# Kernel optimization log

Hardware: AMD Instinct MI355X
Metric: run time of the kernel (lower is better)

Reference implementation:

```python
import jax, jax.numpy as jnp
import numpy as np

N = 100_000   # number of sparse points
C = 128       # channels
K3 = 27       # 3x3x3 kernel offsets


def sparse_conv(x, nbr, W, b):
    """Minkowski-style sparse conv: gather-GEMM-scatter.
    x:   [N, Cin] point features
    nbr: [N, K3] neighbor index per kernel offset; index N -> missing (zero row)
    W:   [K3, Cin, Cout], b: [Cout]
    """
    x_pad = jnp.concatenate([x, jnp.zeros((1, x.shape[1]), x.dtype)], axis=0)

    def step(acc, wk_nk):
        Wk, nk = wk_nk                      # Wk: [Cin,Cout], nk: [N]
        return acc + x_pad[nk] @ Wk, None   # gather + GEMM, accumulate

    acc0 = jnp.broadcast_to(b, (x.shape[0], W.shape[2])).astype(x.dtype)
    acc, _ = jax.lax.scan(step, acc0, (W, nbr.T))
    return acc


def setup_inputs() -> dict:
    key = jax.random.key(0)
    ks = jax.random.split(key, 12)
    Ch = C // 2

    def w(k, shape, fan_in):
        return jax.random.normal(k, shape, dtype=jnp.float32) / np.sqrt(fan_in)

    x = jax.random.normal(ks[0], (N, C), dtype=jnp.float32)
    # neighbor map; value N means "no neighbor" (maps to zero-padded row)
    nbr = jax.random.randint(ks[1], (N, K3), 0, N + 1, dtype=jnp.int32)

    return {
        "x": x,
        "nbr": nbr,
        "W00": w(ks[2], (K3, C, Ch), K3 * C),   # conv0_0: kxkxk, C -> C/2
        "b00": jnp.zeros((Ch,), jnp.float32),
        "W01": w(ks[3], (K3, Ch, Ch), K3 * Ch),  # conv0_1: kxkxk, C/2 -> C/2
        "b01": jnp.zeros((Ch,), jnp.float32),
        "W10": w(ks[4], (C, Ch), C),             # conv1_0: 1x1x1, C -> C/2
        "b10": jnp.zeros((Ch,), jnp.float32),
        "W11": w(ks[5], (K3, Ch, Ch), K3 * Ch),  # conv1_1: kxkxk, C/2 -> C/2
        "b11": jnp.zeros((Ch,), jnp.float32),
        "W12": w(ks[6], (Ch, Ch), Ch),           # conv1_2: 1x1x1, C/2 -> C/2
        "b12": jnp.zeros((Ch,), jnp.float32),
    }


def reference(x, nbr, W00, b00, W01, b01, W10, b10, W11, b11, W12, b12):
    # branch 0: conv -> relu -> conv
    h0 = jax.nn.relu(sparse_conv(x, nbr, W00, b00))
    out0 = sparse_conv(h0, nbr, W01, b01)
    # branch 1: 1x1 conv -> relu -> conv -> relu -> 1x1 conv
    h1 = jax.nn.relu(x @ W10 + b10)
    h1 = jax.nn.relu(sparse_conv(h1, nbr, W11, b11))
    out1 = h1 @ W12 + b12
    # concat channels, residual add
    return jnp.concatenate([out0, out1], axis=1) + x
```

## Files before the change

### kernel.cpp

```cpp
#include <hip/hip_runtime.h>
#include <hip/hip_bf16.h>
#include <stdint.h>

typedef __bf16 bf16x8 __attribute__((ext_vector_type(8)));
typedef float  f32x4  __attribute__((ext_vector_type(4)));

#define MFMA(A, B, C) __builtin_amdgcn_mfma_f32_16x16x32_bf16((A), (B), (C), 0, 0, 0)

static __device__ __forceinline__ unsigned short f2b(float f) {
    union { float f; unsigned int u; } v; v.f = f;
    return (unsigned short)((v.u + 0x7FFFu + ((v.u >> 16) & 1u)) >> 16);
}

static __device__ __forceinline__ bf16x8 perm_frag(int sel, bf16x8 D) {
    union { bf16x8 v; int d[4]; } u, r;
    u.v = D;
#pragma unroll
    for (int w = 0; w < 4; ++w) r.d[w] = __builtin_amdgcn_ds_bpermute(sel, u.d[w]);
    return r.v;
}

__global__ __launch_bounds__(256) void convert_kernel(
    const float* __restrict__ x, unsigned short* __restrict__ xb,
    unsigned short* __restrict__ hb, int N) {
    long long i = (long long)blockIdx.x * blockDim.x + threadIdx.x;
    long long base = i * 4;
    long long nx = (long long)N * 128;
    long long total = nx + 128;
    if (base >= total) return;
    if (base < nx) {
        float4 v = *(const float4*)(x + base);
        ushort4 o;
        o.x = f2b(v.x); o.y = f2b(v.y); o.z = f2b(v.z); o.w = f2b(v.w);
        *(ushort4*)(xb + base) = o;
    } else {
        ushort4 z = make_ushort4(0, 0, 0, 0);
        *(ushort4*)(xb + base) = z;
        *(ushort4*)(hb + base) = z;
    }
}

__global__ __launch_bounds__(256) void pack_kernel(
    const float* __restrict__ W00, const float* __restrict__ W01,
    const float* __restrict__ W10, const float* __restrict__ W11,
    const float* __restrict__ W12,
    unsigned short* __restrict__ wp00, unsigned short* __restrict__ wpC,
    unsigned short* __restrict__ wp10, unsigned short* __restrict__ wp12) {
    int g = blockIdx.x * blockDim.x + threadIdx.x;
    const float* W; int cinSteps; int which;
    if (g < 27648)      { W = W00; cinSteps = 4; which = 0; }
    else if (g < 41472) { g -= 27648; W = W01; cinSteps = 2; which = 1; }
    else if (g < 55296) { g -= 41472; W = W11; cinSteps = 2; which = 2; }
    else if (g < 56320) { g -= 55296; W = W10; cinSteps = 4; which = 3; }
    else if (g < 56832) { g -= 56320; W = W12; cinSteps = 2; which = 4; }
    else return;
    int lane = g & 63;
    int st   = g >> 6;
    int t    = st & 3;
    int s    = st >> 2;
    int q = lane >> 4, n16 = lane & 15;
    int k    = s / cinSteps;
    int cinb = (s % cinSteps) * 32;
    int Cin  = cinSteps * 32;
    int cout = t * 16 + n16;
    unsigned short o[8];
#pragma unroll
    for (int j = 0; j < 8; ++j) {
        float v = W[(size_t)(k * Cin + cinb + q * 8 + j) * 64 + cout];
        o[j] = f2b(v);
    }
    unsigned short* dst;
    if (which == 0)      dst = wp00 + (size_t)g * 8;
    else if (which == 1) dst = wpC + (size_t)k * 8192 +
                               ((size_t)(((s & 1) * 4 + t) * 64 + lane)) * 8;
    else if (which == 2) dst = wpC + (size_t)k * 8192 + 4096 +
                               ((size_t)(((s & 1) * 4 + t) * 64 + lane)) * 8;
    else if (which == 3) dst = wp10 + (size_t)g * 8;
    else                 dst = wp12 + (size_t)g * 8;
    *(ushort4*)(dst)     = make_ushort4(o[0], o[1], o[2], o[3]);
    *(ushort4*)(dst + 4) = make_ushort4(o[4], o[5], o[6], o[7]);
}

__global__ __launch_bounds__(256, 2) void passB_kernel(
    const unsigned short* __restrict__ xb, const int* __restrict__ nbr,
    const unsigned short* __restrict__ wp00, const unsigned short* __restrict__ wp10,
    const float* __restrict__ b00, const float* __restrict__ b10,
    unsigned short* __restrict__ hb, int N) {
    __shared__ __align__(16) unsigned short bbuf[2][8192];
    __shared__ int lds_idx[128 * 27];
    int tid = threadIdx.x;
    int lane = tid & 63;
    int wv   = tid >> 6;
    int q = lane >> 4, n16 = lane & 15;
    int rowq = lane >> 2, chunk = lane & 3;
    int sel = (n16 * 4 + q) * 4;
    int rowbase = blockIdx.x * 128 + wv * 32;

    {
        long long gbase = (long long)blockIdx.x * 128 * 27;
        long long lim = (long long)N * 27 - 1;
        for (int i = tid; i < 3456; i += 256) {
            long long gi = gbase + i; if (gi > lim) gi = lim;
            lds_idx[i] = nbr[gi];
        }
    }
    int4 br[4];
#pragma unroll
    for (int j = 0; j < 4; ++j) br[j] = *(const int4*)(wp00 + j * 2048 + tid * 8);
#pragma unroll
    for (int j = 0; j < 4; ++j) *(int4*)(&bbuf[0][j * 2048 + tid * 8]) = br[j];
    __syncthreads();

    f32x4 acc0[2][4];
    f32x4 acc1[2][4];
#pragma unroll
    for (int rs = 0; rs < 2; ++rs)
#pragma unroll
        for (int t = 0; t < 4; ++t) { acc0[rs][t] = (f32x4)0.f; acc1[rs][t] = (f32x4)0.f; }

    int idxb0 = (wv * 32 + rowq) * 27;
    int idxb1 = (wv * 32 + 16 + rowq) * 27;
    int own0 = min(rowbase + rowq, N - 1);
    int own1 = min(rowbase + 16 + rowq, N - 1);

    int ia = lds_idx[idxb0], ib = lds_idx[idxb1];
    bf16x8 D0[4], D1[4];
    {
        const unsigned short* p0 = xb + (size_t)ia * 128 + chunk * 8;
        const unsigned short* p1 = xb + (size_t)ib * 128 + chunk * 8;
#pragma unroll
        for (int s2 = 0; s2 < 4; ++s2) {
            D0[s2] = *(const bf16x8*)(p0 + s2 * 32);
            D1[s2] = *(const bf16x8*)(p1 + s2 * 32);
        }
    }

    for (int k = 0; k < 27; ++k) {
        int buf = k & 1;
        if (k < 26) {
            const unsigned short* src = wp00 + (size_t)(k + 1) * 8192;
#pragma unroll
            for (int j = 0; j < 4; ++j) br[j] = *(const int4*)(src + j * 2048 + tid * 8);
        }
        int ian = (k + 1 < 27) ? lds_idx[idxb0 + k + 1] : own0;
        int ibn = (k + 1 < 27) ? lds_idx[idxb1 + k + 1] : own1;
        bf16x8 D0n[4], D1n[4];
        {
            const unsigned short* p0 = xb + (size_t)ian * 128 + chunk * 8;
            const unsigned short* p1 = xb + (size_t)ibn * 128 + chunk * 8;
#pragma unroll
            for (int s2 = 0; s2 < 4; ++s2) {
                D0n[s2] = *(const bf16x8*)(p0 + s2 * 32);
                D1n[s2] = *(const bf16x8*)(p1 + s2 * 32);
            }
        }
        const unsigned short* lb = &bbuf[buf][0];
#pragma unroll
        for (int s2 = 0; s2 < 4; ++s2) {
            bf16x8 A0 = perm_frag(sel, D0[s2]);
            bf16x8 A1 = perm_frag(sel, D1[s2]);
#pragma unroll
            for (int t = 0; t < 4; ++t) {
                bf16x8 B = *(const bf16x8*)(lb + (s2 * 4 + t) * 512 + lane * 8);
                acc0[0][t] = MFMA(A0, B, acc0[0][t]);
                acc0[1][t] = MFMA(A1, B, acc0[1][t]);
            }
        }
        if (k < 26) {
#pragma unroll
            for (int j = 0; j < 4; ++j)
                *(int4*)(&bbuf[buf ^ 1][j * 2048 + tid * 8]) = br[j];
        }
#pragma unroll
        for (int s2 = 0; s2 < 4; ++s2) { D0[s2] = D0n[s2]; D1[s2] = D1n[s2]; }
        __syncthreads();
    }

#pragma unroll
    for (int s2 = 0; s2 < 4; ++s2) {
        bf16x8 A0 = perm_frag(sel, D0[s2]);
        bf16x8 A1 = perm_frag(sel, D1[s2]);
#pragma unroll
        for (int t = 0; t < 4; ++t) {
            bf16x8 B = *(const bf16x8*)(wp10 + s2 * 2048 + t * 512 + lane * 8);
            acc1[0][t] = MFMA(A0, B, acc1[0][t]);
            acc1[1][t] = MFMA(A1, B, acc1[1][t]);
        }
    }

#pragma unroll
    for (int rs = 0; rs < 2; ++rs)
#pragma unroll
        for (int t = 0; t < 4; ++t) {
            int col = t * 16 + n16;
            float bb0 = b00[col], bb1 = b10[col];
#pragma unroll
            for (int r = 0; r < 4; ++r) {
                int row = rowbase + rs * 16 + q * 4 + r;
                if (row < N) {
                    hb[(size_t)row * 128 + col]      = f2b(fmaxf(acc0[rs][t][r] + bb0, 0.f));
                    hb[(size_t)row * 128 + 64 + col] = f2b(fmaxf(acc1[rs][t][r] + bb1, 0.f));
                }
            }
        }
}

__global__ __launch_bounds__(256, 2) void passC_kernel(
    const unsigned short* __restrict__ hb, const int* __restrict__ nbr,
    const float* __restrict__ x,
    const unsigned short* __restrict__ wpC, const unsigned short* __restrict__ wp12,
    const float* __restrict__ b01, const float* __restrict__ b11,
    const float* __restrict__ b12, float* __restrict__ out, int N) {
    __shared__ __align__(16) unsigned short bbuf[2][8192];
    __shared__ int lds_idx[128 * 27];
    int tid = threadIdx.x;
    int lane = tid & 63;
    int wv   = tid >> 6;
    int q = lane >> 4, n16 = lane & 15;
    int rowq = lane >> 2, chunk = lane & 3;
    int sel = (n16 * 4 + q) * 4;
    int rowbase = blockIdx.x * 128 + wv * 32;

    {
        long long gbase = (long long)blockIdx.x * 128 * 27;
        long long lim = (long long)N * 27 - 1;
        for (int i = tid; i < 3456; i += 256) {
            long long gi = gbase + i; if (gi > lim) gi = lim;
            lds_idx[i] = nbr[gi];
        }
    }
    int4 br[4];
#pragma unroll
    for (int j = 0; j < 4; ++j) br[j] = *(const int4*)(wpC + j * 2048 + tid * 8);
#pragma unroll
    for (int j = 0; j < 4; ++j) *(int4*)(&bbuf[0][j * 2048 + tid * 8]) = br[j];
    __syncthreads();

    f32x4 accO0[2][4];
    f32x4 accT[2][4];
#pragma unroll
    for (int rs = 0; rs < 2; ++rs)
#pragma unroll
        for (int t = 0; t < 4; ++t) { accO0[rs][t] = (f32x4)0.f; accT[rs][t] = (f32x4)0.f; }

    int idxb0 = (wv * 32 + rowq) * 27;
    int idxb1 = (wv * 32 + 16 + rowq) * 27;

    int ia = lds_idx[idxb0], ib = lds_idx[idxb1];
    bf16x8 DA0[2], DC0[2], DA1[2], DC1[2];
    {
        const unsigned short* p0 = hb + (size_t)ia * 128 + chunk * 8;
        const unsigned short* p1 = hb + (size_t)ib * 128 + chunk * 8;
#pragma unroll
        for (int s2 = 0; s2 < 2; ++s2) {
            DA0[s2] = *(const bf16x8*)(p0 + s2 * 32);
            DC0[s2] = *(const bf16x8*)(p0 + 64 + s2 * 32);
            DA1[s2] = *(const bf16x8*)(p1 + s2 * 32);
            DC1[s2] = *(const bf16x8*)(p1 + 64 + s2 * 32);
        }
    }

    for (int k = 0; k < 27; ++k) {
        int buf = k & 1;
        if (k < 26) {
            const unsigned short* src = wpC + (size_t)(k + 1) * 8192;
#pragma unroll
            for (int j = 0; j < 4; ++j) br[j] = *(const int4*)(src + j * 2048 + tid * 8);
        }
        bf16x8 DA0n[2], DC0n[2], DA1n[2], DC1n[2];
        if (k < 26) {
            int ian = lds_idx[idxb0 + k + 1];
            int ibn = lds_idx[idxb1 + k + 1];
            const unsigned short* p0 = hb + (size_t)ian * 128 + chunk * 8;
            const unsigned short* p1 = hb + (size_t)ibn * 128 + chunk * 8;
#pragma unroll
            for (int s2 = 0; s2 < 2; ++s2) {
                DA0n[s2] = *(const bf16x8*)(p0 + s2 * 32);
                DC0n[s2] = *(const bf16x8*)(p0 + 64 + s2 * 32);
                DA1n[s2] = *(const bf16x8*)(p1 + s2 * 32);
                DC1n[s2] = *(const bf16x8*)(p1 + 64 + s2 * 32);
            }
        }
        const unsigned short* lb = &bbuf[buf][0];
#pragma unroll
        for (int s2 = 0; s2 < 2; ++s2) {
            bf16x8 A0 = perm_frag(sel, DA0[s2]);
            bf16x8 A1 = perm_frag(sel, DA1[s2]);
#pragma unroll
            for (int t = 0; t < 4; ++t) {
                bf16x8 B = *(const bf16x8*)(lb + (s2 * 4 + t) * 512 + lane * 8);
                accO0[0][t] = MFMA(A0, B, accO0[0][t]);
                accO0[1][t] = MFMA(A1, B, accO0[1][t]);
            }
            bf16x8 C0 = perm_frag(sel, DC0[s2]);
            bf16x8 C1 = perm_frag(sel, DC1[s2]);
#pragma unroll
            for (int t = 0; t < 4; ++t) {
                bf16x8 B2 = *(const bf16x8*)(lb + 4096 + (s2 * 4 + t) * 512 + lane * 8);
                accT[0][t] = MFMA(C0, B2, accT[0][t]);
                accT[1][t] = MFMA(C1, B2, accT[1][t]);
            }
        }
        if (k < 26) {
#pragma unroll
            for (int j = 0; j < 4; ++j)
                *(int4*)(&bbuf[buf ^ 1][j * 2048 + tid * 8]) = br[j];
#pragma unroll
            for (int s2 = 0; s2 < 2; ++s2) {
                DA0[s2] = DA0n[s2]; DC0[s2] = DC0n[s2];
                DA1[s2] = DA1n[s2]; DC1[s2] = DC1n[s2];
            }
        }
        __syncthreads();
    }

    unsigned short* scratch = &bbuf[0][0];
    unsigned short* myl = scratch + wv * 2304;
#pragma unroll
    for (int rs = 0; rs < 2; ++rs)
#pragma unroll
        for (int t = 0; t < 4; ++t) {
            int col = t * 16 + n16;
            float bo = b01[col], bt = b11[col];
#pragma unroll
            for (int r = 0; r < 4; ++r) {
                int row = rowbase + rs * 16 + q * 4 + r;
                if (row < N) {
                    float xv = __builtin_nontemporal_load(x + (size_t)row * 128 + col);
                    __builtin_nontemporal_store(accO0[rs][t][r] + bo + xv,
                                                out + (size_t)row * 128 + col);
                }
                float tv = fmaxf(accT[rs][t][r] + bt, 0.f);
                myl[(rs * 16 + q * 4 + r) * 72 + col] = f2b(tv);
            }
        }

    f32x4 accO1[2][4];
#pragma unroll
    for (int rs = 0; rs < 2; ++rs)
#pragma unroll
        for (int t = 0; t < 4; ++t) accO1[rs][t] = (f32x4)0.f;
#pragma unroll
    for (int s2 = 0; s2 < 2; ++s2) {
        bf16x8 A0 = *(const bf16x8*)(myl + n16 * 72 + s2 * 32 + q * 8);
        bf16x8 A1 = *(const bf16x8*)(myl + (16 + n16) * 72 + s2 * 32 + q * 8);
#pragma unroll
        for (int t = 0; t < 4; ++t) {
            bf16x8 B = *(const bf16x8*)(wp12 + s2 * 2048 + t * 512 + lane * 8);
            accO1[0][t] = MFMA(A0, B, accO1[0][t]);
            accO1[1][t] = MFMA(A1, B, accO1[1][t]);
        }
    }
#pragma unroll
    for (int rs = 0; rs < 2; ++rs)
#pragma unroll
        for (int t = 0; t < 4; ++t) {
            int col = t * 16 + n16;
            float bo = b12[col];
#pragma unroll
            for (int r = 0; r < 4; ++r) {
                int row = rowbase + rs * 16 + q * 4 + r;
                if (row < N) {
                    float xv = __builtin_nontemporal_load(x + (size_t)row * 128 + 64 + col);
                    __builtin_nontemporal_store(accO1[rs][t][r] + bo + xv,
                                                out + (size_t)row * 128 + 64 + col);
                }
            }
        }
}

extern "C" void kernel_launch(void* const* d_in, const int* in_sizes, int n_in,
                              void* d_out, int out_size, void* d_ws, size_t ws_size,
                              hipStream_t stream) {
    const float* x   = (const float*)d_in[0];
    const int*   nbr = (const int*)d_in[1];
    const float* W00 = (const float*)d_in[2];
    const float* b00 = (const float*)d_in[3];
    const float* W01 = (const float*)d_in[4];
    const float* b01 = (const float*)d_in[5];
    const float* W10 = (const float*)d_in[6];
    const float* b10 = (const float*)d_in[7];
    const float* W11 = (const float*)d_in[8];
    const float* b11 = (const float*)d_in[9];
    const float* W12 = (const float*)d_in[10];
    const float* b12 = (const float*)d_in[11];
    float* out = (float*)d_out;
    int N = in_sizes[0] / 128;

    char* ws = (char*)d_ws;
    size_t cur = 0;
    unsigned short* xb  = (unsigned short*)(ws + cur); cur += (size_t)(N + 1) * 128 * 2;
    unsigned short* hb  = (unsigned short*)(ws + cur); cur += (size_t)(N + 1) * 128 * 2;
    unsigned short* wp00 = (unsigned short*)(ws + cur); cur += 27648 * 8 * 2;
    unsigned short* wpC  = (unsigned short*)(ws + cur); cur += (size_t)27 * 8192 * 2;
    unsigned short* wp10 = (unsigned short*)(ws + cur); cur += 8192 * 2;
    unsigned short* wp12 = (unsigned short*)(ws + cur); cur += 4096 * 2;

    long long cvt_groups = ((long long)N * 128 + 128) / 4;
    int cvt_blocks = (int)((cvt_groups + 255) / 256);
    convert_kernel<<<cvt_blocks, 256, 0, stream>>>(x, xb, hb, N);
    pack_kernel<<<222, 256, 0, stream>>>(W00, W01, W10, W11, W12,
                                         wp00, wpC, wp10, wp12);
    int blocks = (N + 127) / 128;
    passB_kernel<<<blocks, 256, 0, stream>>>(xb, nbr, wp00, wp10, b00, b10, hb, N);
    passC_kernel<<<blocks, 256, 0, stream>>>(hb, nbr, x, wpC, wp12,
                                             b01, b11, b12, out, N);
}
```

Before: 414.3 us.

## Convert gather-GEMM passes to persistent blocks with atomic strip scheduling

Both conv passes now launch a fixed grid of 768 persistent blocks that pull 128-row strips from a global atomic counter, instead of one block per strip. The in-loop __syncthreads is also replaced with an explicit lgkmcnt wait plus s_barrier, so the barrier no longer waits on outstanding global loads. The aim is to cut block launch and tail overhead and to overlap the gather prefetch with the barrier. In exchange it adds an atomic and an extra barrier per strip, and it reloads the first weight slice for every strip.

```diff
diff --git a/kernel.cpp b/kernel.cpp
--- a/kernel.cpp
+++ b/kernel.cpp
@@ -6,6 +6,8 @@
 typedef float  f32x4  __attribute__((ext_vector_type(4)));
 
 #define MFMA(A, B, C) __builtin_amdgcn_mfma_f32_16x16x32_bf16((A), (B), (C), 0, 0, 0)
+
+#define LDS_BARRIER() asm volatile("s_waitcnt lgkmcnt(0)\n\ts_barrier" ::: "memory")
 
 static __device__ __forceinline__ unsigned short f2b(float f) {
     union { float f; unsigned int u; } v; v.f = f;
@@ -85,124 +87,133 @@
     const unsigned short* __restrict__ xb, const int* __restrict__ nbr,
     const unsigned short* __restrict__ wp00, const unsigned short* __restrict__ wp10,
     const float* __restrict__ b00, const float* __restrict__ b10,
-    unsigned short* __restrict__ hb, int N) {
+    unsigned short* __restrict__ hb, int N, int* __restrict__ ctr, int nstrips) {
     __shared__ __align__(16) unsigned short bbuf[2][8192];
     __shared__ int lds_idx[128 * 27];
+    __shared__ int sstrip;
     int tid = threadIdx.x;
     int lane = tid & 63;
     int wv   = tid >> 6;
     int q = lane >> 4, n16 = lane & 15;
     int rowq = lane >> 2, chunk = lane & 3;
     int sel = (n16 * 4 + q) * 4;
-    int rowbase = blockIdx.x * 128 + wv * 32;
-
-    {
-        long long gbase = (long long)blockIdx.x * 128 * 27;
-        long long lim = (long long)N * 27 - 1;
-        for (int i = tid; i < 3456; i += 256) {
-            long long gi = gbase + i; if (gi > lim) gi = lim;
-            lds_idx[i] = nbr[gi];
-        }
-    }
-    int4 br[4];
-#pragma unroll
-    for (int j = 0; j < 4; ++j) br[j] = *(const int4*)(wp00 + j * 2048 + tid * 8);
-#pragma unroll
-    for (int j = 0; j < 4; ++j) *(int4*)(&bbuf[0][j * 2048 + tid * 8]) = br[j];
-    __syncthreads();
-
-    f32x4 acc0[2][4];
-    f32x4 acc1[2][4];
-#pragma unroll
-    for (int rs = 0; rs < 2; ++rs)
-#pragma unroll
-        for (int t = 0; t < 4; ++t) { acc0[rs][t] = (f32x4)0.f; acc1[rs][t] = (f32x4)0.f; }
-
-    int idxb0 = (wv * 32 + rowq) * 27;
-    int idxb1 = (wv * 32 + 16 + rowq) * 27;
-    int own0 = min(rowbase + rowq, N - 1);
-    int own1 = min(rowbase + 16 + rowq, N - 1);
-
-    int ia = lds_idx[idxb0], ib = lds_idx[idxb1];
-    bf16x8 D0[4], D1[4];
-    {
-        const unsigned short* p0 = xb + (size_t)ia * 128 + chunk * 8;
-        const unsigned short* p1 = xb + (size_t)ib * 128 + chunk * 8;
-#pragma unroll
-        for (int s2 = 0; s2 < 4; ++s2) {
-            D0[s2] = *(const bf16x8*)(p0 + s2 * 32);
-            D1[s2] = *(const bf16x8*)(p1 + s2 * 32);
-        }
-    }
-
-    for (int k = 0; k < 27; ++k) {
-        int buf = k & 1;
-        if (k < 26) {
-            const unsigned short* src = wp00 + (size_t)(k + 1) * 8192;
-#pragma unroll
-            for (int j = 0; j < 4; ++j) br[j] = *(const int4*)(src + j * 2048 + tid * 8);
-        }
-        int ian = (k + 1 < 27) ? lds_idx[idxb0 + k + 1] : own0;
-        int ibn = (k + 1 < 27) ? lds_idx[idxb1 + k + 1] : own1;
-        bf16x8 D0n[4], D1n[4];
+
+    for (;;) {
+        if (tid == 0) sstrip = atomicAdd(ctr, 1);
+        __syncthreads();
+        int strip = sstrip;
+        if (strip >= nstrips) break;
+        int rowbase = strip * 128 + wv * 32;
+
+        int4 br[4];
+#pragma unroll
+        for (int j = 0; j < 4; ++j) br[j] = *(const int4*)(wp00 + j * 2048 + tid * 8);
         {
-            const unsigned short* p0 = xb + (size_t)ian * 128 + chunk * 8;
-            const unsigned short* p1 = xb + (size_t)ibn * 128 + chunk * 8;
+            long long gbase = (long long)strip * 128 * 27;
+            long long lim = (long long)N * 27 - 1;
+            for (int i = tid; i < 3456; i += 256) {
+                long long gi = gbase + i; if (gi > lim) gi = lim;
+                lds_idx[i] = nbr[gi];
+            }
+        }
+#pragma unroll
+        for (int j = 0; j < 4; ++j) *(int4*)(&bbuf[0][j * 2048 + tid * 8]) = br[j];
+        __syncthreads();
+
+        f32x4 acc0[2][4];
+        f32x4 acc1[2][4];
+#pragma unroll
+        for (int rs = 0; rs < 2; ++rs)
+#pragma unroll
+            for (int t = 0; t < 4; ++t) { acc0[rs][t] = (f32x4)0.f; acc1[rs][t] = (f32x4)0.f; }
+
+        int idxb0 = (wv * 32 + rowq) * 27;
+        int idxb1 = (wv * 32 + 16 + rowq) * 27;
+        int own0 = min(rowbase + rowq, N - 1);
+        int own1 = min(rowbase + 16 + rowq, N - 1);
+
+        int ia = lds_idx[idxb0], ib = lds_idx[idxb1];
+        bf16x8 D0[4], D1[4];
+        {
+            const unsigned short* p0 = xb + (size_t)ia * 128 + chunk * 8;
+            const unsigned short* p1 = xb + (size_t)ib * 128 + chunk * 8;
 #pragma unroll
             for (int s2 = 0; s2 < 4; ++s2) {
-                D0n[s2] = *(const bf16x8*)(p0 + s2 * 32);
-                D1n[s2] = *(const bf16x8*)(p1 + s2 * 32);
-            }
-        }
-        const unsigned short* lb = &bbuf[buf][0];
+                D0[s2] = *(const bf16x8*)(p0 + s2 * 32);
+                D1[s2] = *(const bf16x8*)(p1 + s2 * 32);
+            }
+        }
+
+        for (int k = 0; k < 27; ++k) {
+            int buf = k & 1;
+            if (k < 26) {
+                const unsigned short* src = wp00 + (size_t)(k + 1) * 8192;
+#pragma unroll
+                for (int j = 0; j < 4; ++j) br[j] = *(const int4*)(src + j * 2048 + tid * 8);
+            }
+            int ian = (k + 1 < 27) ? lds_idx[idxb0 + k + 1] : own0;
+            int ibn = (k + 1 < 27) ? lds_idx[idxb1 + k + 1] : own1;
+            bf16x8 D0n[4], D1n[4];
+            {
+                const unsigned short* p0 = xb + (size_t)ian * 128 + chunk * 8;
+                const unsigned short* p1 = xb + (size_t)ibn * 128 + chunk * 8;
+#pragma unroll
+                for (int s2 = 0; s2 < 4; ++s2) {
+                    D0n[s2] = *(const bf16x8*)(p0 + s2 * 32);
+                    D1n[s2] = *(const bf16x8*)(p1 + s2 * 32);
+                }
+            }
+            const unsigned short* lb = &bbuf[buf][0];
+#pragma unroll
+            for (int s2 = 0; s2 < 4; ++s2) {
+                bf16x8 A0 = perm_frag(sel, D0[s2]);
+                bf16x8 A1 = perm_frag(sel, D1[s2]);
+#pragma unroll
+                for (int t = 0; t < 4; ++t) {
+                    bf16x8 B = *(const bf16x8*)(lb + (s2 * 4 + t) * 512 + lane * 8);
+                    acc0[0][t] = MFMA(A0, B, acc0[0][t]);
+                    acc0[1][t] = MFMA(A1, B, acc0[1][t]);
+                }
+            }
+            if (k < 26) {
+#pragma unroll
+                for (int j = 0; j < 4; ++j)
+                    *(int4*)(&bbuf[buf ^ 1][j * 2048 + tid * 8]) = br[j];
+            }
+#pragma unroll
+            for (int s2 = 0; s2 < 4; ++s2) { D0[s2] = D0n[s2]; D1[s2] = D1n[s2]; }
+            LDS_BARRIER();
+        }
+
 #pragma unroll
         for (int s2 = 0; s2 < 4; ++s2) {
             bf16x8 A0 = perm_frag(sel, D0[s2]);
             bf16x8 A1 = perm_frag(sel, D1[s2]);
 #pragma unroll
             for (int t = 0; t < 4; ++t) {
-                bf16x8 B = *(const bf16x8*)(lb + (s2 * 4 + t) * 512 + lane * 8);
-                acc0[0][t] = MFMA(A0, B, acc0[0][t]);
-                acc0[1][t] = MFMA(A1, B, acc0[1][t]);
-            }
-        }
-        if (k < 26) {
-#pragma unroll
-            for (int j = 0; j < 4; ++j)
-                *(int4*)(&bbuf[buf ^ 1][j * 2048 + tid * 8]) = br[j];
-        }
-#pragma unroll
-        for (int s2 = 0; s2 < 4; ++s2) { D0[s2] = D0n[s2]; D1[s2] = D1n[s2]; }
+                bf16x8 B = *(const bf16x8*)(wp10 + s2 * 2048 + t * 512 + lane * 8);
+                acc1[0][t] = MFMA(A0, B, acc1[0][t]);
+                acc1[1][t] = MFMA(A1, B, acc1[1][t]);
+            }
+        }
+
+#pragma unroll
+        for (int rs = 0; rs < 2; ++rs)
+#pragma unroll
+            for (int t = 0; t < 4; ++t) {
+                int col = t * 16 + n16;
+                float bb0 = b00[col], bb1 = b10[col];
+#pragma unroll
+                for (int r = 0; r < 4; ++r) {
+                    int row = rowbase + rs * 16 + q * 4 + r;
+                    if (row < N) {
+                        hb[(size_t)row * 128 + col]      = f2b(fmaxf(acc0[rs][t][r] + bb0, 0.f));
+                        hb[(size_t)row * 128 + 64 + col] = f2b(fmaxf(acc1[rs][t][r] + bb1, 0.f));
+                    }
+                }
+            }
         __syncthreads();
     }
-
-#pragma unroll
-    for (int s2 = 0; s2 < 4; ++s2) {
-        bf16x8 A0 = perm_frag(sel, D0[s2]);
-        bf16x8 A1 = perm_frag(sel, D1[s2]);
-#pragma unroll
-        for (int t = 0; t < 4; ++t) {
-            bf16x8 B = *(const bf16x8*)(wp10 + s2 * 2048 + t * 512 + lane * 8);
-            acc1[0][t] = MFMA(A0, B, acc1[0][t]);
-            acc1[1][t] = MFMA(A1, B, acc1[1][t]);
-        }
-    }
-
-#pragma unroll
-    for (int rs = 0; rs < 2; ++rs)
-#pragma unroll
-        for (int t = 0; t < 4; ++t) {
-            int col = t * 16 + n16;
-            float bb0 = b00[col], bb1 = b10[col];
-#pragma unroll
-            for (int r = 0; r < 4; ++r) {
-                int row = rowbase + rs * 16 + q * 4 + r;
-                if (row < N) {
-                    hb[(size_t)row * 128 + col]      = f2b(fmaxf(acc0[rs][t][r] + bb0, 0.f));
-                    hb[(size_t)row * 128 + 64 + col] = f2b(fmaxf(acc1[rs][t][r] + bb1, 0.f));
-                }
-            }
-        }
 }
 
 __global__ __launch_bounds__(256, 2) void passC_kernel(
@@ -210,163 +221,173 @@
     const float* __restrict__ x,
     const unsigned short* __restrict__ wpC, const unsigned short* __restrict__ wp12,
     const float* __restrict__ b01, const float* __restrict__ b11,
-    const float* __restrict__ b12, float* __restrict__ out, int N) {
+    const float* __restrict__ b12, float* __restrict__ out, int N,
+    int* __restrict__ ctr, int nstrips) {
     __shared__ __align__(16) unsigned short bbuf[2][8192];
     __shared__ int lds_idx[128 * 27];
+    __shared__ int sstrip;
     int tid = threadIdx.x;
     int lane = tid & 63;
     int wv   = tid >> 6;
     int q = lane >> 4, n16 = lane & 15;
     int rowq = lane >> 2, chunk = lane & 3;
     int sel = (n16 * 4 + q) * 4;
-    int rowbase = blockIdx.x * 128 + wv * 32;
-
-    {
-        long long gbase = (long long)blockIdx.x * 128 * 27;
-        long long lim = (long long)N * 27 - 1;
-        for (int i = tid; i < 3456; i += 256) {
-            long long gi = gbase + i; if (gi > lim) gi = lim;
-            lds_idx[i] = nbr[gi];
-        }
+
+    for (;;) {
+        if (tid == 0) sstrip = atomicAdd(ctr, 1);
+        __syncthreads();
+        int strip = sstrip;
+        if (strip >= nstrips) break;
+        int rowbase = strip * 128 + wv * 32;
+
+        int4 br[4];
+#pragma unroll
+        for (int j = 0; j < 4; ++j) br[j] = *(const int4*)(wpC + j * 2048 + tid * 8);
+        {
+            long long gbase = (long long)strip * 128 * 27;
+            long long lim = (long long)N * 27 - 1;
+            for (int i = tid; i < 3456; i += 256) {
+                long long gi = gbase + i; if (gi > lim) gi = lim;
+                lds_idx[i] = nbr[gi];
+            }
+        }
+#pragma unroll
+        for (int j = 0; j < 4; ++j) *(int4*)(&bbuf[0][j * 2048 + tid * 8]) = br[j];
+        __syncthreads();
+
+        f32x4 accO0[2][4];
+        f32x4 accT[2][4];
+#pragma unroll
+        for (int rs = 0; rs < 2; ++rs)
+#pragma unroll
+            for (int t = 0; t < 4; ++t) { accO0[rs][t] = (f32x4)0.f; accT[rs][t] = (f32x4)0.f; }
+
+        int idxb0 = (wv * 32 + rowq) * 27;
+        int idxb1 = (wv * 32 + 16 + rowq) * 27;
+
+        int ia = lds_idx[idxb0], ib = lds_idx[idxb1];
+        bf16x8 DA0[2], DC0[2], DA1[2], DC1[2];
+        {
+            const unsigned short* p0 = hb + (size_t)ia * 128 + chunk * 8;
+            const unsigned short* p1 = hb + (size_t)ib * 128 + chunk * 8;
+#pragma unroll
+            for (int s2 = 0; s2 < 2; ++s2) {
+                DA0[s2] = *(const bf16x8*)(p0 + s2 * 32);
+                DC0[s2] = *(const bf16x8*)(p0 + 64 + s2 * 32);
+                DA1[s2] = *(const bf16x8*)(p1 + s2 * 32);
+                DC1[s2] = *(const bf16x8*)(p1 + 64 + s2 * 32);
+            }
+        }
+
+        for (int k = 0; k < 27; ++k) {
+            int buf = k & 1;
+            if (k < 26) {
+                const unsigned short* src = wpC + (size_t)(k + 1) * 8192;
+#pragma unroll
+                for (int j = 0; j < 4; ++j) br[j] = *(const int4*)(src + j * 2048 + tid * 8);
+            }
+            bf16x8 DA0n[2], DC0n[2], DA1n[2], DC1n[2];
+            if (k < 26) {
+                int ian = lds_idx[idxb0 + k + 1];
+                int ibn = lds_idx[idxb1 + k + 1];
+                const unsigned short* p0 = hb + (size_t)ian * 128 + chunk * 8;
+                const unsigned short* p1 = hb + (size_t)ibn * 128 + chunk * 8;
+#pragma unroll
+                for (int s2 = 0; s2 < 2; ++s2) {
+                    DA0n[s2] = *(const bf16x8*)(p0 + s2 * 32);
+                    DC0n[s2] = *(const bf16x8*)(p0 + 64 + s2 * 32);
+                    DA1n[s2] = *(const bf16x8*)(p1 + s2 * 32);
+                    DC1n[s2] = *(const bf16x8*)(p1 + 64 + s2 * 32);
+                }
+            }
+            const unsigned short* lb = &bbuf[buf][0];
+#pragma unroll
+            for (int s2 = 0; s2 < 2; ++s2) {
+                bf16x8 A0 = perm_frag(sel, DA0[s2]);
+                bf16x8 A1 = perm_frag(sel, DA1[s2]);
+#pragma unroll
+                for (int t = 0; t < 4; ++t) {
+                    bf16x8 B = *(const bf16x8*)(lb + (s2 * 4 + t) * 512 + lane * 8);
+                    accO0[0][t] = MFMA(A0, B, accO0[0][t]);
+                    accO0[1][t] = MFMA(A1, B, accO0[1][t]);
+                }
+                bf16x8 C0 = perm_frag(sel, DC0[s2]);
+                bf16x8 C1 = perm_frag(sel, DC1[s2]);
+#pragma unroll
+                for (int t = 0; t < 4; ++t) {
+                    bf16x8 B2 = *(const bf16x8*)(lb + 4096 + (s2 * 4 + t) * 512 + lane * 8);
+                    accT[0][t] = MFMA(C0, B2, accT[0][t]);
+                    accT[1][t] = MFMA(C1, B2, accT[1][t]);
+                }
+            }
+            if (k < 26) {
+#pragma unroll
+                for (int j = 0; j < 4; ++j)
+                    *(int4*)(&bbuf[buf ^ 1][j * 2048 + tid * 8]) = br[j];
+#pragma unroll
+                for (int s2 = 0; s2 < 2; ++s2) {
+                    DA0[s2] = DA0n[s2]; DC0[s2] = DC0n[s2];
+                    DA1[s2] = DA1n[s2]; DC1[s2] = DC1n[s2];
+                }
+            }
+            LDS_BARRIER();
+        }
+
+        unsigned short* scratch = &bbuf[0][0];
+        unsigned short* myl = scratch + wv * 2304;
+#pragma unroll
+        for (int rs = 0; rs < 2; ++rs)
+#pragma unroll
+            for (int t = 0; t < 4; ++t) {
+                int col = t * 16 + n16;
+                float bo = b01[col], bt = b11[col];
+#pragma unroll
+                for (int r = 0; r < 4; ++r) {
+                    int row = rowbase + rs * 16 + q * 4 + r;
+                    if (row < N) {
+                        float xv = __builtin_nontemporal_load(x + (size_t)row * 128 + col);
+                        __builtin_nontemporal_store(accO0[rs][t][r] + bo + xv,
+                                                    out + (size_t)row * 128 + col);
+                    }
+                    float tv = fmaxf(accT[rs][t][r] + bt, 0.f);
+                    myl[(rs * 16 + q * 4 + r) * 72 + col] = f2b(tv);
+                }
+            }
+
+        f32x4 accO1[2][4];
+#pragma unroll
+        for (int rs = 0; rs < 2; ++rs)
+#pragma unroll
+            for (int t = 0; t < 4; ++t) accO1[rs][t] = (f32x4)0.f;
+#pragma unroll
+        for (int s2 = 0; s2 < 2; ++s2) {
+            bf16x8 A0 = *(const bf16x8*)(myl + n16 * 72 + s2 * 32 + q * 8);
+            bf16x8 A1 = *(const bf16x8*)(myl + (16 + n16) * 72 + s2 * 32 + q * 8);
+#pragma unroll
+            for (int t = 0; t < 4; ++t) {
+                bf16x8 B = *(const bf16x8*)(wp12 + s2 * 2048 + t * 512 + lane * 8);
+                accO1[0][t] = MFMA(A0, B, accO1[0][t]);
+                accO1[1][t] = MFMA(A1, B, accO1[1][t]);
+            }
+        }
+#pragma unroll
+        for (int rs = 0; rs < 2; ++rs)
+#pragma unroll
+            for (int t = 0; t < 4; ++t) {
+                int col = t * 16 + n16;
+                float bo = b12[col];
+#pragma unroll
+                for (int r = 0; r < 4; ++r) {
+                    int row = rowbase + rs * 16 + q * 4 + r;
+                    if (row < N) {
+                        float xv = __builtin_nontemporal_load(x + (size_t)row * 128 + 64 + col);
+                        __builtin_nontemporal_store(accO1[rs][t][r] + bo + xv,
+                                                    out + (size_t)row * 128 + 64 + col);
+                    }
+                }
+            }
+        __syncthreads();
     }
-    int4 br[4];
-#pragma unroll
-    for (int j = 0; j < 4; ++j) br[j] = *(const int4*)(wpC + j * 2048 + tid * 8);
-#pragma unroll
-    for (int j = 0; j < 4; ++j) *(int4*)(&bbuf[0][j * 2048 + tid * 8]) = br[j];
-    __syncthreads();
-
-    f32x4 accO0[2][4];
-    f32x4 accT[2][4];
-#pragma unroll
-    for (int rs = 0; rs < 2; ++rs)
-#pragma unroll
-        for (int t = 0; t < 4; ++t) { accO0[rs][t] = (f32x4)0.f; accT[rs][t] = (f32x4)0.f; }
-
-    int idxb0 = (wv * 32 + rowq) * 27;
-    int idxb1 = (wv * 32 + 16 + rowq) * 27;
-
-    int ia = lds_idx[idxb0], ib = lds_idx[idxb1];
-    bf16x8 DA0[2], DC0[2], DA1[2], DC1[2];
-    {
-        const unsigned short* p0 = hb + (size_t)ia * 128 + chunk * 8;
-        const unsigned short* p1 = hb + (size_t)ib * 128 + chunk * 8;
-#pragma unroll
-        for (int s2 = 0; s2 < 2; ++s2) {
-            DA0[s2] = *(const bf16x8*)(p0 + s2 * 32);
-            DC0[s2] = *(const bf16x8*)(p0 + 64 + s2 * 32);
-            DA1[s2] = *(const bf16x8*)(p1 + s2 * 32);
-            DC1[s2] = *(const bf16x8*)(p1 + 64 + s2 * 32);
-        }
-    }
-
-    for (int k = 0; k < 27; ++k) {
-        int buf = k & 1;
-        if (k < 26) {
-            const unsigned short* src = wpC + (size_t)(k + 1) * 8192;
-#pragma unroll
-            for (int j = 0; j < 4; ++j) br[j] = *(const int4*)(src + j * 2048 + tid * 8);
-        }
-        bf16x8 DA0n[2], DC0n[2], DA1n[2], DC1n[2];
-        if (k < 26) {
-            int ian = lds_idx[idxb0 + k + 1];
-            int ibn = lds_idx[idxb1 + k + 1];
-            const unsigned short* p0 = hb + (size_t)ian * 128 + chunk * 8;
-            const unsigned short* p1 = hb + (size_t)ibn * 128 + chunk * 8;
-#pragma unroll
-            for (int s2 = 0; s2 < 2; ++s2) {
-                DA0n[s2] = *(const bf16x8*)(p0 + s2 * 32);
-                DC0n[s2] = *(const bf16x8*)(p0 + 64 + s2 * 32);
-                DA1n[s2] = *(const bf16x8*)(p1 + s2 * 32);
-                DC1n[s2] = *(const bf16x8*)(p1 + 64 + s2 * 32);
-            }
-        }
-        const unsigned short* lb = &bbuf[buf][0];
-#pragma unroll
-        for (int s2 = 0; s2 < 2; ++s2) {
-            bf16x8 A0 = perm_frag(sel, DA0[s2]);
-            bf16x8 A1 = perm_frag(sel, DA1[s2]);
-#pragma unroll
-            for (int t = 0; t < 4; ++t) {
-                bf16x8 B = *(const bf16x8*)(lb + (s2 * 4 + t) * 512 + lane * 8);
-                accO0[0][t] = MFMA(A0, B, accO0[0][t]);
-                accO0[1][t] = MFMA(A1, B, accO0[1][t]);
-            }
-            bf16x8 C0 = perm_frag(sel, DC0[s2]);
-            bf16x8 C1 = perm_frag(sel, DC1[s2]);
-#pragma unroll
-            for (int t = 0; t < 4; ++t) {
-                bf16x8 B2 = *(const bf16x8*)(lb + 4096 + (s2 * 4 + t) * 512 + lane * 8);
-                accT[0][t] = MFMA(C0, B2, accT[0][t]);
-                accT[1][t] = MFMA(C1, B2, accT[1][t]);
-            }
-        }
-        if (k < 26) {
-#pragma unroll
-            for (int j = 0; j < 4; ++j)
-                *(int4*)(&bbuf[buf ^ 1][j * 2048 + tid * 8]) = br[j];
-#pragma unroll
-            for (int s2 = 0; s2 < 2; ++s2) {
-                DA0[s2] = DA0n[s2]; DC0[s2] = DC0n[s2];
-                DA1[s2] = DA1n[s2]; DC1[s2] = DC1n[s2];
-            }
-        }
-        __syncthreads();
-    }
-
-    unsigned short* scratch = &bbuf[0][0];
-    unsigned short* myl = scratch + wv * 2304;
-#pragma unroll
-    for (int rs = 0; rs < 2; ++rs)
-#pragma unroll
-        for (int t = 0; t < 4; ++t) {
-            int col = t * 16 + n16;
-            float bo = b01[col], bt = b11[col];
-#pragma unroll
-            for (int r = 0; r < 4; ++r) {
-                int row = rowbase + rs * 16 + q * 4 + r;
-                if (row < N) {
-                    float xv = __builtin_nontemporal_load(x + (size_t)row * 128 + col);
-                    __builtin_nontemporal_store(accO0[rs][t][r] + bo + xv,
-                                                out + (size_t)row * 128 + col);
-                }
-                float tv = fmaxf(accT[rs][t][r] + bt, 0.f);
-                myl[(rs * 16 + q * 4 + r) * 72 + col] = f2b(tv);
-            }
-        }
-
-    f32x4 accO1[2][4];
-#pragma unroll
-    for (int rs = 0; rs < 2; ++rs)
-#pragma unroll
-        for (int t = 0; t < 4; ++t) accO1[rs][t] = (f32x4)0.f;
-#pragma unroll
-    for (int s2 = 0; s2 < 2; ++s2) {
-        bf16x8 A0 = *(const bf16x8*)(myl + n16 * 72 + s2 * 32 + q * 8);
-        bf16x8 A1 = *(const bf16x8*)(myl + (16 + n16) * 72 + s2 * 32 + q * 8);
-#pragma unroll
-        for (int t = 0; t < 4; ++t) {
-            bf16x8 B = *(const bf16x8*)(wp12 + s2 * 2048 + t * 512 + lane * 8);
-            accO1[0][t] = MFMA(A0, B, accO1[0][t]);
-            accO1[1][t] = MFMA(A1, B, accO1[1][t]);
-        }
-    }
-#pragma unroll
-    for (int rs = 0; rs < 2; ++rs)
-#pragma unroll
-        for (int t = 0; t < 4; ++t) {
-            int col = t * 16 + n16;
-            float bo = b12[col];
-#pragma unroll
-            for (int r = 0; r < 4; ++r) {
-                int row = rowbase + rs * 16 + q * 4 + r;
-                if (row < N) {
-                    float xv = __builtin_nontemporal_load(x + (size_t)row * 128 + 64 + col);
-                    __builtin_nontemporal_store(accO1[rs][t][r] + bo + xv,
-                                                out + (size_t)row * 128 + 64 + col);
-                }
-            }
-        }
 }
 
 extern "C" void kernel_launch(void* const* d_in, const int* in_sizes, int n_in,
@@ -395,14 +416,19 @@
     unsigned short* wpC  = (unsigned short*)(ws + cur); cur += (size_t)27 * 8192 * 2;
     unsigned short* wp10 = (unsigned short*)(ws + cur); cur += 8192 * 2;
     unsigned short* wp12 = (unsigned short*)(ws + cur); cur += 4096 * 2;
-
+    cur = (cur + 255) & ~(size_t)255;
+    int* ctrs = (int*)(ws + cur); cur += 256;
+
+    hipMemsetAsync(ctrs, 0, 8, stream);
     long long cvt_groups = ((long long)N * 128 + 128) / 4;
     int cvt_blocks = (int)((cvt_groups + 255) / 256);
     convert_kernel<<<cvt_blocks, 256, 0, stream>>>(x, xb, hb, N);
     pack_kernel<<<222, 256, 0, stream>>>(W00, W01, W10, W11, W12,
                                          wp00, wpC, wp10, wp12);
-    int blocks = (N + 127) / 128;
-    passB_kernel<<<blocks, 256, 0, stream>>>(xb, nbr, wp00, wp10, b00, b10, hb, N);
-    passC_kernel<<<blocks, 256, 0, stream>>>(hb, nbr, x, wpC, wp12,
-                                             b01, b11, b12, out, N);
-}
+    int nstrips = (N + 127) / 128;
+    passB_kernel<<<768, 256, 0, stream>>>(xb, nbr, wp00, wp10, b00, b10, hb, N,
+                                          ctrs + 0, nstrips);
+    passC_kernel<<<768, 256, 0, stream>>>(hb, nbr, x, wpC, wp12,
+                                          b01, b11, b12, out, N,
+                                          ctrs + 1, nstrips);
+}
```

Result: no change. 412.0 us (-0.5%).

## Read packed weights directly from global memory, drop LDS double-buffer and barriers

Applied to the files above, without the earlier changes.

Removes the LDS double-buffered weight staging and the per-offset __syncthreads in both sparse-conv passes. Each wave now reads its MFMA B fragments straight from the pre-packed global weight arrays, relying on L1/L2 caching, which cuts LDS use and may raise occupancy. It also merges the convert and pack kernels into one launch and adds nontemporal hints on the neighbor-index loads and hb stores. The trade-off is more global/L2 traffic per wave in place of LDS reuse across the four waves of a block.

```diff
diff --git a/kernel.cpp b/kernel.cpp
--- a/kernel.cpp
+++ b/kernel.cpp
@@ -20,33 +20,33 @@
     return r.v;
 }
 
-__global__ __launch_bounds__(256) void convert_kernel(
+__global__ __launch_bounds__(256) void prep_kernel(
     const float* __restrict__ x, unsigned short* __restrict__ xb,
-    unsigned short* __restrict__ hb, int N) {
-    long long i = (long long)blockIdx.x * blockDim.x + threadIdx.x;
-    long long base = i * 4;
-    long long nx = (long long)N * 128;
-    long long total = nx + 128;
-    if (base >= total) return;
-    if (base < nx) {
-        float4 v = *(const float4*)(x + base);
-        ushort4 o;
-        o.x = f2b(v.x); o.y = f2b(v.y); o.z = f2b(v.z); o.w = f2b(v.w);
-        *(ushort4*)(xb + base) = o;
-    } else {
-        ushort4 z = make_ushort4(0, 0, 0, 0);
-        *(ushort4*)(xb + base) = z;
-        *(ushort4*)(hb + base) = z;
-    }
-}
-
-__global__ __launch_bounds__(256) void pack_kernel(
+    unsigned short* __restrict__ hb, int N, int cvtBlocks,
     const float* __restrict__ W00, const float* __restrict__ W01,
     const float* __restrict__ W10, const float* __restrict__ W11,
     const float* __restrict__ W12,
     unsigned short* __restrict__ wp00, unsigned short* __restrict__ wpC,
     unsigned short* __restrict__ wp10, unsigned short* __restrict__ wp12) {
-    int g = blockIdx.x * blockDim.x + threadIdx.x;
+    if (blockIdx.x < (unsigned)cvtBlocks) {
+        long long i = (long long)blockIdx.x * blockDim.x + threadIdx.x;
+        long long base = i * 4;
+        long long nx = (long long)N * 128;
+        long long total = nx + 128;
+        if (base >= total) return;
+        if (base < nx) {
+            float4 v = *(const float4*)(x + base);
+            ushort4 o;
+            o.x = f2b(v.x); o.y = f2b(v.y); o.z = f2b(v.z); o.w = f2b(v.w);
+            *(ushort4*)(xb + base) = o;
+        } else {
+            ushort4 z = make_ushort4(0, 0, 0, 0);
+            *(ushort4*)(xb + base) = z;
+            *(ushort4*)(hb + base) = z;
+        }
+        return;
+    }
+    int g = (blockIdx.x - cvtBlocks) * blockDim.x + threadIdx.x;
     const float* W; int cinSteps; int which;
     if (g < 27648)      { W = W00; cinSteps = 4; which = 0; }
     else if (g < 41472) { g -= 27648; W = W01; cinSteps = 2; which = 1; }
@@ -86,7 +86,6 @@
     const unsigned short* __restrict__ wp00, const unsigned short* __restrict__ wp10,
     const float* __restrict__ b00, const float* __restrict__ b10,
     unsigned short* __restrict__ hb, int N) {
-    __shared__ __align__(16) unsigned short bbuf[2][8192];
     __shared__ int lds_idx[128 * 27];
     int tid = threadIdx.x;
     int lane = tid & 63;
@@ -101,14 +100,9 @@
         long long lim = (long long)N * 27 - 1;
         for (int i = tid; i < 3456; i += 256) {
             long long gi = gbase + i; if (gi > lim) gi = lim;
-            lds_idx[i] = nbr[gi];
-        }
-    }
-    int4 br[4];
-#pragma unroll
-    for (int j = 0; j < 4; ++j) br[j] = *(const int4*)(wp00 + j * 2048 + tid * 8);
-#pragma unroll
-    for (int j = 0; j < 4; ++j) *(int4*)(&bbuf[0][j * 2048 + tid * 8]) = br[j];
+            lds_idx[i] = __builtin_nontemporal_load(nbr + gi);
+        }
+    }
     __syncthreads();
 
     f32x4 acc0[2][4];
@@ -136,12 +130,6 @@
     }
 
     for (int k = 0; k < 27; ++k) {
-        int buf = k & 1;
-        if (k < 26) {
-            const unsigned short* src = wp00 + (size_t)(k + 1) * 8192;
-#pragma unroll
-            for (int j = 0; j < 4; ++j) br[j] = *(const int4*)(src + j * 2048 + tid * 8);
-        }
         int ian = (k + 1 < 27) ? lds_idx[idxb0 + k + 1] : own0;
         int ibn = (k + 1 < 27) ? lds_idx[idxb1 + k + 1] : own1;
         bf16x8 D0n[4], D1n[4];
@@ -154,26 +142,20 @@
                 D1n[s2] = *(const bf16x8*)(p1 + s2 * 32);
             }
         }
-        const unsigned short* lb = &bbuf[buf][0];
+        const unsigned short* bp = wp00 + (size_t)k * 8192 + lane * 8;
 #pragma unroll
         for (int s2 = 0; s2 < 4; ++s2) {
             bf16x8 A0 = perm_frag(sel, D0[s2]);
             bf16x8 A1 = perm_frag(sel, D1[s2]);
 #pragma unroll
             for (int t = 0; t < 4; ++t) {
-                bf16x8 B = *(const bf16x8*)(lb + (s2 * 4 + t) * 512 + lane * 8);
+                bf16x8 B = *(const bf16x8*)(bp + s2 * 2048 + t * 512);
                 acc0[0][t] = MFMA(A0, B, acc0[0][t]);
                 acc0[1][t] = MFMA(A1, B, acc0[1][t]);
             }
         }
-        if (k < 26) {
-#pragma unroll
-            for (int j = 0; j < 4; ++j)
-                *(int4*)(&bbuf[buf ^ 1][j * 2048 + tid * 8]) = br[j];
-        }
 #pragma unroll
         for (int s2 = 0; s2 < 4; ++s2) { D0[s2] = D0n[s2]; D1[s2] = D1n[s2]; }
-        __syncthreads();
     }
 
 #pragma unroll
@@ -198,8 +180,12 @@
             for (int r = 0; r < 4; ++r) {
                 int row = rowbase + rs * 16 + q * 4 + r;
                 if (row < N) {
-                    hb[(size_t)row * 128 + col]      = f2b(fmaxf(acc0[rs][t][r] + bb0, 0.f));
-                    hb[(size_t)row * 128 + 64 + col] = f2b(fmaxf(acc1[rs][t][r] + bb1, 0.f));
+                    __builtin_nontemporal_store(
+                        f2b(fmaxf(acc0[rs][t][r] + bb0, 0.f)),
+                        hb + (size_t)row * 128 + col);
+                    __builtin_nontemporal_store(
+                        f2b(fmaxf(acc1[rs][t][r] + bb1, 0.f)),
+                        hb + (size_t)row * 128 + 64 + col);
                 }
             }
         }
@@ -211,8 +197,8 @@
     const unsigned short* __restrict__ wpC, const unsigned short* __restrict__ wp12,
     const float* __restrict__ b01, const float* __restrict__ b11,
     const float* __restrict__ b12, float* __restrict__ out, int N) {
-    __shared__ __align__(16) unsigned short bbuf[2][8192];
     __shared__ int lds_idx[128 * 27];
+    __shared__ __align__(16) unsigned short scratch[4 * 2304];
     int tid = threadIdx.x;
     int lane = tid & 63;
     int wv   = tid >> 6;
@@ -226,14 +212,9 @@
         long long lim = (long long)N * 27 - 1;
         for (int i = tid; i < 3456; i += 256) {
             long long gi = gbase + i; if (gi > lim) gi = lim;
-            lds_idx[i] = nbr[gi];
-        }
-    }
-    int4 br[4];
-#pragma unroll
-    for (int j = 0; j < 4; ++j) br[j] = *(const int4*)(wpC + j * 2048 + tid * 8);
-#pragma unroll
-    for (int j = 0; j < 4; ++j) *(int4*)(&bbuf[0][j * 2048 + tid * 8]) = br[j];
+            lds_idx[i] = __builtin_nontemporal_load(nbr + gi);
+        }
+    }
     __syncthreads();
 
     f32x4 accO0[2][4];
@@ -261,12 +242,6 @@
     }
 
     for (int k = 0; k < 27; ++k) {
-        int buf = k & 1;
-        if (k < 26) {
-            const unsigned short* src = wpC + (size_t)(k + 1) * 8192;
-#pragma unroll
-            for (int j = 0; j < 4; ++j) br[j] = *(const int4*)(src + j * 2048 + tid * 8);
-        }
         bf16x8 DA0n[2], DC0n[2], DA1n[2], DC1n[2];
         if (k < 26) {
             int ian = lds_idx[idxb0 + k + 1];
@@ -281,14 +256,14 @@
                 DC1n[s2] = *(const bf16x8*)(p1 + 64 + s2 * 32);
             }
         }
-        const unsigned short* lb = &bbuf[buf][0];
+        const unsigned short* bp = wpC + (size_t)k * 8192 + lane * 8;
 #pragma unroll
         for (int s2 = 0; s2 < 2; ++s2) {
             bf16x8 A0 = perm_frag(sel, DA0[s2]);
             bf16x8 A1 = perm_frag(sel, DA1[s2]);
 #pragma unroll
             for (int t = 0; t < 4; ++t) {
-                bf16x8 B = *(const bf16x8*)(lb + (s2 * 4 + t) * 512 + lane * 8);
+                bf16x8 B = *(const bf16x8*)(bp + (s2 * 4 + t) * 512);
                 accO0[0][t] = MFMA(A0, B, accO0[0][t]);
                 accO0[1][t] = MFMA(A1, B, accO0[1][t]);
             }
@@ -296,25 +271,20 @@
             bf16x8 C1 = perm_frag(sel, DC1[s2]);
 #pragma unroll
             for (int t = 0; t < 4; ++t) {
-                bf16x8 B2 = *(const bf16x8*)(lb + 4096 + (s2 * 4 + t) * 512 + lane * 8);
+                bf16x8 B2 = *(const bf16x8*)(bp + 4096 + (s2 * 4 + t) * 512);
                 accT[0][t] = MFMA(C0, B2, accT[0][t]);
                 accT[1][t] = MFMA(C1, B2, accT[1][t]);
             }
         }
         if (k < 26) {
-#pragma unroll
-            for (int j = 0; j < 4; ++j)
-                *(int4*)(&bbuf[buf ^ 1][j * 2048 + tid * 8]) = br[j];
 #pragma unroll
             for (int s2 = 0; s2 < 2; ++s2) {
                 DA0[s2] = DA0n[s2]; DC0[s2] = DC0n[s2];
                 DA1[s2] = DA1n[s2]; DC1[s2] = DC1n[s2];
             }
         }
-        __syncthreads();
-    }
-
-    unsigned short* scratch = &bbuf[0][0];
+    }
+
     unsigned short* myl = scratch + wv * 2304;
 #pragma unroll
     for (int rs = 0; rs < 2; ++rs)
@@ -398,9 +368,9 @@
 
     long long cvt_groups = ((long long)N * 128 + 128) / 4;
     int cvt_blocks = (int)((cvt_groups + 255) / 256);
-    convert_kernel<<<cvt_blocks, 256, 0, stream>>>(x, xb, hb, N);
-    pack_kernel<<<222, 256, 0, stream>>>(W00, W01, W10, W11, W12,
-                                         wp00, wpC, wp10, wp12);
+    prep_kernel<<<cvt_blocks + 222, 256, 0, stream>>>(
+        x, xb, hb, N, cvt_blocks,
+        W00, W01, W10, W11, W12, wp00, wpC, wp10, wp12);
     int blocks = (N + 127) / 128;
     passB_kernel<<<blocks, 256, 0, stream>>>(xb, nbr, wp00, wp10, b00, b10, hb, N);
     passC_kernel<<<blocks, 256, 0, stream>>>(hb, nbr, x, wpC, wp12,
```

New measurement: 427.4 us. 1.03x slower.
